# Optimization experiments

Hardware: AMD Instinct MI355X
Metric: run time of the kernel (lower is better)

Reference implementation:

```python
import jax, jax.numpy as jnp
import numpy as np

K = 50          # number of negative samples (init arg k)
GAMMA = 1.0     # margin (init arg gamma)
CHUNK = 32      # anchor-row chunk for cdist to bound memory


def cdist_l1(queries, base):
    """Pairwise cityblock distance [A, N] computed in chunks over queries."""
    A, d = queries.shape
    q = queries.reshape(A // CHUNK, CHUNK, d)

    def body(carry, q_chunk):
        # [CHUNK, N]
        dist = jnp.sum(jnp.abs(q_chunk[:, None, :] - base[None, :, :]), axis=-1)
        return carry, dist

    _, dists = jax.lax.scan(body, None, q)
    return dists.reshape(A, base.shape[0])


def setup_inputs() -> dict:
    key = jax.random.key(0)
    k1, k2, k3, k4 = jax.random.split(key, 4)
    N, d, A = 20000, 128, 1024
    return {
        "out1": jax.random.normal(k1, (N, d), dtype=jnp.float32),
        "out2": jax.random.normal(k2, (N, d), dtype=jnp.float32),
        "anchor1": jax.random.randint(k3, (A,), 0, N, dtype=jnp.int64),
        "anchor2": jax.random.randint(k4, (A,), 0, N, dtype=jnp.int64),
    }


def reference(out1, out2, anchor1, anchor2):
    ae1 = out1[anchor1]  # [A, d]
    ae2 = out2[anchor2]  # [A, d]

    # Negative sampling (torch does this on detached numpy arrays):
    # k nearest (smallest L1 distance) candidates in the other graph.
    o1s = jax.lax.stop_gradient(out1)
    o2s = jax.lax.stop_gradient(out2)
    dist1 = cdist_l1(jax.lax.stop_gradient(ae1), o2s)  # [A, N]
    dist2 = cdist_l1(jax.lax.stop_gradient(ae2), o1s)  # [A, N]
    _, neg_idx1 = jax.lax.top_k(-dist1, K)  # [A, K] indices into out2
    _, neg_idx2 = jax.lax.top_k(-dist2, K)  # [A, K] indices into out1

    neg1 = out2[neg_idx1]  # [A, K, d]
    neg2 = out1[neg_idx2]  # [A, K, d]

    pos = jnp.sum(jnp.abs(ae1 - ae2), axis=1)  # [A]
    D = pos + GAMMA

    B1 = -jnp.sum(jnp.abs(ae1[:, None, :] - neg1), axis=2)  # [A, K]
    L1 = jnp.sum(jax.nn.relu(D[:, None] + B1))
    B2 = -jnp.sum(jnp.abs(ae2[:, None, :] - neg2), axis=2)  # [A, K]
    L2 = jnp.sum(jax.nn.relu(D[:, None] + B2))

    return (L1 + L2) / (anchor1.shape[0] * K)
```

## Files before the change

kernel.cpp:

```cpp
#include <hip/hip_runtime.h>
#include <hip/hip_bf16.h>

#define NPTS  20000
#define DIM   128
#define NA    1024
#define NTASK 2048
#define G     8
#define P     4
#define TILE  1024
#define NTILE 20
#define NBX   (NTASK / G)
#define NWG   (NBX * NTILE)
#define SLOT  96
#define KSEL  50
#define GAMMA 1.0f
#define RRANK 12
#define LMAX  (NTILE * SLOT)
#define MFIX  8.0f
#define SQF   (255.0f / (2.0f * MFIX))
#define DQF   (2.0f * MFIX / 255.0f)
#define PRE_A (2 * NPTS * 8)
#define PRE_B (NTASK * 8)
#define PRE_N (PRE_A + PRE_B + 256)

typedef unsigned char  u8t;
typedef unsigned short u16t;

static __device__ __forceinline__ unsigned sad8(unsigned a, unsigned b, unsigned c) {
#if __has_builtin(__builtin_amdgcn_sad_u8)
    return __builtin_amdgcn_sad_u8(a, b, c);
#else
    unsigned d;
    asm("v_sad_u8 %0, %1, %2, %3" : "=v"(d) : "v"(a), "v"(b), "v"(c));
    return d;
#endif
}

static __device__ __forceinline__ unsigned q4(const float4 v, const float s) {
    unsigned u0 = __float2uint_rn(fminf(fmaxf((v.x + MFIX) * s, 0.0f), 255.0f));
    unsigned u1 = __float2uint_rn(fminf(fmaxf((v.y + MFIX) * s, 0.0f), 255.0f));
    unsigned u2 = __float2uint_rn(fminf(fmaxf((v.z + MFIX) * s, 0.0f), 255.0f));
    unsigned u3 = __float2uint_rn(fminf(fmaxf((v.w + MFIX) * s, 0.0f), 255.0f));
    return u0 | (u1 << 8) | (u2 << 16) | (u3 << 24);
}

__global__ __launch_bounds__(256) void prep_kernel(
    const float* __restrict__ o1, const float* __restrict__ o2,
    const int* __restrict__ anchor1, const int* __restrict__ anchor2,
    uint4* __restrict__ qp1, uint4* __restrict__ qp2,
    uint4* __restrict__ astage, float* __restrict__ out)
{
    const int idx = (int)blockIdx.x * 256 + (int)threadIdx.x;
    if (idx < PRE_A) {
        const int m  = idx / (NPTS * 8);
        const int r  = idx - m * (NPTS * 8);
        const int n  = r >> 3;
        const int cq = r & 7;
        const float4* src = (const float4*)((m ? o2 : o1) + (size_t)n * DIM + cq * 16);
        uint4 o;
        o.x = q4(src[0], SQF); o.y = q4(src[1], SQF);
        o.z = q4(src[2], SQF); o.w = q4(src[3], SQF);
        (m ? qp2 : qp1)[(size_t)cq * NPTS + n] = o;
    } else if (idx < PRE_A + PRE_B) {
        const int j = idx - PRE_A;
        const int t = j >> 3, cq = j & 7;
        int row; const float* src;
        if (t < NA) { row = anchor1[t];      src = o1; }
        else        { row = anchor2[t - NA]; src = o2; }
        const float4* rp = (const float4*)(src + (size_t)row * DIM + cq * 16);
        uint4 o;
        o.x = q4(rp[0], SQF); o.y = q4(rp[1], SQF);
        o.z = q4(rp[2], SQF); o.w = q4(rp[3], SQF);
        astage[(size_t)cq * NTASK + t] = o;
    } else if (idx == PRE_A + PRE_B) {
        out[0] = 0.0f;
    }
}

__global__ __launch_bounds__(256) void sample_kernel(
    const uint4* __restrict__ qp1, const uint4* __restrict__ qp2,
    const uint4* __restrict__ astage, unsigned* __restrict__ tau)
{
    __shared__ unsigned h[256], scn[256];
    __shared__ unsigned s_b0, s_r1;

    const int tid = threadIdx.x;
    const int t = (int)blockIdx.x;
    const uint4* qp = (t < NA) ? qp2 : qp1;

    uint4 A[8];
    #pragma unroll
    for (int cq = 0; cq < 8; ++cq) A[cq] = astage[(size_t)cq * NTASK + t];

    unsigned d[2];
    #pragma unroll
    for (int k = 0; k < 2; ++k) {
        const int s = tid + k * 256;
        const int n = (s >> 6) * 2500 + (s & 63);
        unsigned acc = 0;
        #pragma unroll
        for (int cq = 0; cq < 8; ++cq) {
            const uint4 pv = qp[(size_t)cq * NPTS + n];
            acc = sad8(pv.x, A[cq].x, acc); acc = sad8(pv.y, A[cq].y, acc);
            acc = sad8(pv.z, A[cq].z, acc); acc = sad8(pv.w, A[cq].w, acc);
        }
        d[k] = acc;
    }
    h[tid] = 0u;
    __syncthreads();
    atomicAdd(&h[d[0] >> 8], 1u);
    atomicAdd(&h[d[1] >> 8], 1u);
    __syncthreads();
    scn[tid] = h[tid];
    __syncthreads();
    for (int off = 1; off < 256; off <<= 1) {
        const unsigned v = scn[tid];
        const unsigned u = (tid >= off) ? scn[tid - off] : 0u;
        __syncthreads();
        scn[tid] = v + u;
        __syncthreads();
    }
    {
        const unsigned cumb = tid ? scn[tid - 1] : 0u;
        if (cumb < RRANK && scn[tid] >= RRANK) { s_b0 = (unsigned)tid; s_r1 = RRANK - cumb; }
    }
    __syncthreads();
    const unsigned b0 = s_b0, r1 = s_r1;
    h[tid] = 0u;
    __syncthreads();
    if ((d[0] >> 8) == b0) atomicAdd(&h[d[0] & 255u], 1u);
    if ((d[1] >> 8) == b0) atomicAdd(&h[d[1] & 255u], 1u);
    __syncthreads();
    scn[tid] = h[tid];
    __syncthreads();
    for (int off = 1; off < 256; off <<= 1) {
        const unsigned v = scn[tid];
        const unsigned u = (tid >= off) ? scn[tid - off] : 0u;
        __syncthreads();
        scn[tid] = v + u;
        __syncthreads();
    }
    {
        const unsigned cumb = tid ? scn[tid - 1] : 0u;
        if (cumb < r1 && scn[tid] >= r1) tau[t] = (b0 << 8) | (unsigned)tid;
    }
}

__global__ __launch_bounds__(256, 8) void dist_kernel(
    const uint4* __restrict__ qp1, const uint4* __restrict__ qp2,
    const uint4* __restrict__ astage, const unsigned* __restrict__ tau,
    u16t* __restrict__ cand, unsigned* __restrict__ bcnt)
{
    __shared__ unsigned scnt[G];

    const int tid = threadIdx.x;
    const int bid = (int)blockIdx.x;
    const int swz = (bid & 7) * (NWG / 8) + (bid >> 3);
    const int tile = swz / NBX;
    const int bx   = swz - tile * NBX;
    const int t0 = bx * G;
    const uint4* qp = (t0 < NA) ? qp2 : qp1;

    if (tid < G) scnt[tid] = 0u;

    const int w = tid >> 6, l = tid & 63;
    const int nbase = tile * TILE + w * 256 + l;

    unsigned acc[P][G];
    #pragma unroll
    for (int p = 0; p < P; ++p)
        #pragma unroll
        for (int g = 0; g < G; ++g) acc[p][g] = 0u;

    #pragma unroll
    for (int cq = 0; cq < 8; ++cq) {
        uint4 A[G];
        #pragma unroll
        for (int g = 0; g < G; ++g) A[g] = astage[(size_t)cq * NTASK + t0 + g];
        uint4 pv[P];
        #pragma unroll
        for (int p = 0; p < P; ++p) {
            int n = nbase + p * 64;
            n = n < NPTS ? n : NPTS - 1;
            pv[p] = qp[(size_t)cq * NPTS + n];
        }
        #pragma unroll
        for (int g = 0; g < G; ++g) {
            #pragma unroll
            for (int p = 0; p < P; ++p) {
                unsigned a = acc[p][g];
                a = sad8(pv[p].x, A[g].x, a);
                a = sad8(pv[p].y, A[g].y, a);
                a = sad8(pv[p].z, A[g].z, a);
                a = sad8(pv[p].w, A[g].w, a);
                acc[p][g] = a;
            }
        }
    }
    __syncthreads();

    #pragma unroll
    for (int g = 0; g < G; ++g) {
        const unsigned tg = tau[t0 + g];
        u16t* cg = cand + (size_t)(t0 + g) * LMAX + tile * SLOT;
        #pragma unroll
        for (int p = 0; p < P; ++p) {
            const int n = nbase + p * 64;
            if (n < NPTS && acc[p][g] <= tg) {
                const unsigned idx = atomicAdd(&scnt[g], 1u);
                if (idx < SLOT) cg[idx] = (u16t)acc[p][g];
            }
        }
    }
    __syncthreads();
    if (tid < G) bcnt[(size_t)(t0 + tid) * NTILE + tile] = scnt[tid];
}

__global__ __launch_bounds__(256) void finish_kernel(
    const float* __restrict__ o1, const float* __restrict__ o2,
    const int* __restrict__ anchor1, const int* __restrict__ anchor2,
    const uint4* __restrict__ qp1, const uint4* __restrict__ qp2,
    const uint4* __restrict__ astage,
    const u16t* __restrict__ cand, const unsigned* __restrict__ bcnt,
    float* __restrict__ d_out)
{
    __shared__ float red[256];
    __shared__ unsigned h[256], scn[256];
    __shared__ unsigned cnts[NTILE];
    __shared__ unsigned s_b0, s_r1, s_bad;

    const int tid = threadIdx.x;
    const int t = (int)blockIdx.x;

    const int a = (t < NA) ? t : (t - NA);
    const int i1 = anchor1[a], i2 = anchor2[a];
    float p = 0.0f;
    if (tid < DIM) p = fabsf(o1[(size_t)i1 * DIM + tid] - o2[(size_t)i2 * DIM + tid]);
    red[tid] = p;
    __syncthreads();
    for (int s = 128; s >= 1; s >>= 1) { if (tid < s) red[tid] += red[tid + s]; __syncthreads(); }
    const float D = red[0] + GAMMA;
    __syncthreads();

    if (tid < NTILE) cnts[tid] = bcnt[(size_t)t * NTILE + tid];
    __syncthreads();
    if (tid == 0) {
        unsigned total = 0, bad = 0;
        for (int i = 0; i < NTILE; ++i) { if (cnts[i] > SLOT) bad = 1; total += cnts[i]; }
        s_bad = bad | (total < KSEL ? 1u : 0u);
    }
    h[tid] = 0u;
    __syncthreads();

    float local = 0.0f;
    unsigned kth, remf;

    if (!s_bad) {
        const unsigned* c32 = (const unsigned*)(cand + (size_t)t * LMAX);
        unsigned val[8];
        #pragma unroll
        for (int k = 0; k < 4; ++k) {
            const int i32 = tid + k * 256;
            unsigned v0 = 0xFFFFu, v1 = 0xFFFFu;
            if (i32 < LMAX / 2) {
                const unsigned wv = c32[i32];
                const int tile = i32 / (SLOT / 2);
                const int j0 = 2 * i32 - tile * SLOT;
                const unsigned cn = cnts[tile];
                if ((unsigned)j0 < cn)       v0 = wv & 0xFFFFu;
                if ((unsigned)(j0 + 1) < cn) v1 = wv >> 16;
            }
            val[2 * k] = v0; val[2 * k + 1] = v1;
            if (v0 != 0xFFFFu) atomicAdd(&h[v0 >> 8], 1u);
            if (v1 != 0xFFFFu) atomicAdd(&h[v1 >> 8], 1u);
        }
        __syncthreads();
        scn[tid] = h[tid];
        __syncthreads();
        for (int off = 1; off < 256; off <<= 1) {
            const unsigned v = scn[tid];
            const unsigned u = (tid >= off) ? scn[tid - off] : 0u;
            __syncthreads();
            scn[tid] = v + u;
            __syncthreads();
        }
        {
            const unsigned cumb = tid ? scn[tid - 1] : 0u;
            if (cumb < KSEL && scn[tid] >= KSEL) { s_b0 = (unsigned)tid; s_r1 = KSEL - cumb; }
        }
        __syncthreads();
        const unsigned b0 = s_b0, r1 = s_r1;
        h[tid] = 0u;
        __syncthreads();
        #pragma unroll
        for (int k = 0; k < 8; ++k)
            if ((val[k] >> 8) == b0) atomicAdd(&h[val[k] & 255u], 1u);
        __syncthreads();
        scn[tid] = h[tid];
        __syncthreads();
        for (int off = 1; off < 256; off <<= 1) {
            const unsigned v = scn[tid];
            const unsigned u = (tid >= off) ? scn[tid - off] : 0u;
            __syncthreads();
            scn[tid] = v + u;
            __syncthreads();
        }
        {
            const unsigned cumb = tid ? scn[tid - 1] : 0u;
            if (cumb < r1 && scn[tid] >= r1) { s_b0 = (unsigned)tid; s_r1 = r1 - cumb; }
        }
        __syncthreads();
        kth = (b0 << 8) | s_b0;
        remf = s_r1;
        #pragma unroll
        for (int k = 0; k < 8; ++k) {
            const unsigned u = val[k];
            if (u < kth) local += fmaxf(D - (float)u * DQF, 0.0f);
        }
    } else {
        const uint4* qp = (t < NA) ? qp2 : qp1;
        uint4 A[8];
        #pragma unroll
        for (int cq = 0; cq < 8; ++cq) A[cq] = astage[(size_t)cq * NTASK + t];
        for (int n = tid; n < NPTS; n += 256) {
            unsigned acc = 0;
            #pragma unroll
            for (int cq = 0; cq < 8; ++cq) {
                const uint4 pv = qp[(size_t)cq * NPTS + n];
                acc = sad8(pv.x, A[cq].x, acc); acc = sad8(pv.y, A[cq].y, acc);
                acc = sad8(pv.z, A[cq].z, acc); acc = sad8(pv.w, A[cq].w, acc);
            }
            atomicAdd(&h[acc >> 8], 1u);
        }
        __syncthreads();
        scn[tid] = h[tid];
        __syncthreads();
        for (int off = 1; off < 256; off <<= 1) {
            const unsigned v = scn[tid];
            const unsigned u = (tid >= off) ? scn[tid - off] : 0u;
            __syncthreads();
            scn[tid] = v + u;
            __syncthreads();
        }
        {
            const unsigned cumb = tid ? scn[tid - 1] : 0u;
            if (cumb < KSEL && scn[tid] >= KSEL) { s_b0 = (unsigned)tid; s_r1 = KSEL - cumb; }
        }
        __syncthreads();
        const unsigned b0 = s_b0, r1 = s_r1;
        h[tid] = 0u;
        __syncthreads();
        for (int n = tid; n < NPTS; n += 256) {
            unsigned acc = 0;
            #pragma unroll
            for (int cq = 0; cq < 8; ++cq) {
                const uint4 pv = qp[(size_t)cq * NPTS + n];
                acc = sad8(pv.x, A[cq].x, acc); acc = sad8(pv.y, A[cq].y, acc);
                acc = sad8(pv.z, A[cq].z, acc); acc = sad8(pv.w, A[cq].w, acc);
            }
            if ((acc >> 8) == b0) atomicAdd(&h[acc & 255u], 1u);
        }
        __syncthreads();
        scn[tid] = h[tid];
        __syncthreads();
        for (int off = 1; off < 256; off <<= 1) {
            const unsigned v = scn[tid];
            const unsigned u = (tid >= off) ? scn[tid - off] : 0u;
            __syncthreads();
            scn[tid] = v + u;
            __syncthreads();
        }
        {
            const unsigned cumb = tid ? scn[tid - 1] : 0u;
            if (cumb < r1 && scn[tid] >= r1) { s_b0 = (unsigned)tid; s_r1 = r1 - cumb; }
        }
        __syncthreads();
        kth = (b0 << 8) | s_b0;
        remf = s_r1;
        for (int n = tid; n < NPTS; n += 256) {
            unsigned acc = 0;
            #pragma unroll
            for (int cq = 0; cq < 8; ++cq) {
                const uint4 pv = qp[(size_t)cq * NPTS + n];
                acc = sad8(pv.x, A[cq].x, acc); acc = sad8(pv.y, A[cq].y, acc);
                acc = sad8(pv.z, A[cq].z, acc); acc = sad8(pv.w, A[cq].w, acc);
            }
            if (acc < kth) local += fmaxf(D - (float)acc * DQF, 0.0f);
        }
    }

    red[tid] = local;
    __syncthreads();
    for (int s = 128; s >= 1; s >>= 1) { if (tid < s) red[tid] += red[tid + s]; __syncthreads(); }
    if (tid == 0) {
        const float total_l = red[0] + (float)remf * fmaxf(D - (float)kth * DQF, 0.0f);
        atomicAdd(d_out, total_l * (1.0f / ((float)NA * (float)KSEL)));
    }
}

extern "C" void kernel_launch(void* const* d_in, const int* in_sizes, int n_in,
                              void* d_out, int out_size, void* d_ws, size_t ws_size,
                              hipStream_t stream) {
    const float* o1 = (const float*)d_in[0];
    const float* o2 = (const float*)d_in[1];
    const int*   a1 = (const int*)d_in[2];
    const int*   a2 = (const int*)d_in[3];
    float* out = (float*)d_out;

    const size_t qbytes = (size_t)NPTS * DIM;
    const size_t abytes = (size_t)NTASK * DIM;
    const uintptr_t end = ((uintptr_t)d_ws + ws_size) & ~(uintptr_t)15;
    unsigned* tau    = (unsigned*)(end - (size_t)NTASK * 4);
    unsigned* bcnt   = (unsigned*)((uintptr_t)tau - (size_t)NTASK * NTILE * 4);
    uint4*    astage = (uint4*)((uintptr_t)bcnt - abytes);
    uint4*    qp2    = (uint4*)((uintptr_t)astage - qbytes);
    uint4*    qp1    = (uint4*)((uintptr_t)qp2 - qbytes);
    u16t*     cand   = (u16t*)d_ws;

    prep_kernel<<<(PRE_N + 255) / 256, 256, 0, stream>>>(
        o1, o2, a1, a2, qp1, qp2, astage, out);
    sample_kernel<<<NTASK, 256, 0, stream>>>(qp1, qp2, astage, tau);
    dist_kernel<<<NWG, 256, 0, stream>>>(qp1, qp2, astage, tau, cand, bcnt);
    finish_kernel<<<NTASK, 256, 0, stream>>>(o1, o2, a1, a2, qp1, qp2, astage,
                                             cand, bcnt, out);
}
```

Baseline: 110.9 us.

## Fuse quantization prep into sampling kernel by quantizing sample rows on the fly

Merges the prep kernel and the sample kernel into one launch. Extra blocks do the quantization while the sampling blocks quantize their anchor and sampled base rows directly from the float inputs, so sampling no longer waits on the prep output. This removes one launch and the serialization between the two stages, at the cost of redundant quantization arithmetic and wider float reads in the sampling blocks. A second, small change in finish_kernel only loads a candidate word when at least one of its two slots is valid.

```diff
diff --git a/kernel.cpp b/kernel.cpp
--- a/kernel.cpp
+++ b/kernel.cpp
@@ -22,6 +22,8 @@
 #define PRE_A (2 * NPTS * 8)
 #define PRE_B (NTASK * 8)
 #define PRE_N (PRE_A + PRE_B + 256)
+#define PBLK  ((PRE_N + 255) / 256)
+#define FUSED (NTASK + PBLK)
 
 typedef unsigned char  u8t;
 typedef unsigned short u16t;
@@ -44,63 +46,78 @@
     return u0 | (u1 << 8) | (u2 << 16) | (u3 << 24);
 }
 
-__global__ __launch_bounds__(256) void prep_kernel(
+__global__ __launch_bounds__(256) void prep_sample_kernel(
     const float* __restrict__ o1, const float* __restrict__ o2,
     const int* __restrict__ anchor1, const int* __restrict__ anchor2,
     uint4* __restrict__ qp1, uint4* __restrict__ qp2,
-    uint4* __restrict__ astage, float* __restrict__ out)
-{
-    const int idx = (int)blockIdx.x * 256 + (int)threadIdx.x;
-    if (idx < PRE_A) {
-        const int m  = idx / (NPTS * 8);
-        const int r  = idx - m * (NPTS * 8);
-        const int n  = r >> 3;
-        const int cq = r & 7;
-        const float4* src = (const float4*)((m ? o2 : o1) + (size_t)n * DIM + cq * 16);
-        uint4 o;
-        o.x = q4(src[0], SQF); o.y = q4(src[1], SQF);
-        o.z = q4(src[2], SQF); o.w = q4(src[3], SQF);
-        (m ? qp2 : qp1)[(size_t)cq * NPTS + n] = o;
-    } else if (idx < PRE_A + PRE_B) {
-        const int j = idx - PRE_A;
-        const int t = j >> 3, cq = j & 7;
-        int row; const float* src;
-        if (t < NA) { row = anchor1[t];      src = o1; }
-        else        { row = anchor2[t - NA]; src = o2; }
-        const float4* rp = (const float4*)(src + (size_t)row * DIM + cq * 16);
-        uint4 o;
-        o.x = q4(rp[0], SQF); o.y = q4(rp[1], SQF);
-        o.z = q4(rp[2], SQF); o.w = q4(rp[3], SQF);
-        astage[(size_t)cq * NTASK + t] = o;
-    } else if (idx == PRE_A + PRE_B) {
-        out[0] = 0.0f;
-    }
-}
-
-__global__ __launch_bounds__(256) void sample_kernel(
-    const uint4* __restrict__ qp1, const uint4* __restrict__ qp2,
-    const uint4* __restrict__ astage, unsigned* __restrict__ tau)
+    uint4* __restrict__ astage, unsigned* __restrict__ tau,
+    float* __restrict__ out)
 {
     __shared__ unsigned h[256], scn[256];
     __shared__ unsigned s_b0, s_r1;
 
     const int tid = threadIdx.x;
-    const int t = (int)blockIdx.x;
-    const uint4* qp = (t < NA) ? qp2 : qp1;
-
+    const int bid = (int)blockIdx.x;
+
+    if (bid >= NTASK) {
+        const int idx = (bid - NTASK) * 256 + tid;
+        if (idx < PRE_A) {
+            const int m  = idx / (NPTS * 8);
+            const int r  = idx - m * (NPTS * 8);
+            const int n  = r >> 3;
+            const int cq = r & 7;
+            const float4* src = (const float4*)((m ? o2 : o1) + (size_t)n * DIM + cq * 16);
+            uint4 o;
+            o.x = q4(src[0], SQF); o.y = q4(src[1], SQF);
+            o.z = q4(src[2], SQF); o.w = q4(src[3], SQF);
+            (m ? qp2 : qp1)[(size_t)cq * NPTS + n] = o;
+        } else if (idx < PRE_A + PRE_B) {
+            const int j = idx - PRE_A;
+            const int t = j >> 3, cq = j & 7;
+            int row; const float* src;
+            if (t < NA) { row = anchor1[t];      src = o1; }
+            else        { row = anchor2[t - NA]; src = o2; }
+            const float4* rp = (const float4*)(src + (size_t)row * DIM + cq * 16);
+            uint4 o;
+            o.x = q4(rp[0], SQF); o.y = q4(rp[1], SQF);
+            o.z = q4(rp[2], SQF); o.w = q4(rp[3], SQF);
+            astage[(size_t)cq * NTASK + t] = o;
+        } else if (idx == PRE_A + PRE_B) {
+            out[0] = 0.0f;
+        }
+        return;
+    }
+
+    const int t = bid;
+    const float* base = (t < NA) ? o2 : o1;
+
+    int row; const float* asrc;
+    if (t < NA) { row = anchor1[t];      asrc = o1; }
+    else        { row = anchor2[t - NA]; asrc = o2; }
+    const float4* ap = (const float4*)(asrc + (size_t)row * DIM);
     uint4 A[8];
     #pragma unroll
-    for (int cq = 0; cq < 8; ++cq) A[cq] = astage[(size_t)cq * NTASK + t];
+    for (int cq = 0; cq < 8; ++cq) {
+        A[cq].x = q4(ap[4 * cq + 0], SQF);
+        A[cq].y = q4(ap[4 * cq + 1], SQF);
+        A[cq].z = q4(ap[4 * cq + 2], SQF);
+        A[cq].w = q4(ap[4 * cq + 3], SQF);
+    }
 
     unsigned d[2];
     #pragma unroll
     for (int k = 0; k < 2; ++k) {
         const int s = tid + k * 256;
         const int n = (s >> 6) * 2500 + (s & 63);
+        const float4* rp = (const float4*)(base + (size_t)n * DIM);
         unsigned acc = 0;
         #pragma unroll
         for (int cq = 0; cq < 8; ++cq) {
-            const uint4 pv = qp[(size_t)cq * NPTS + n];
+            uint4 pv;
+            pv.x = q4(rp[4 * cq + 0], SQF);
+            pv.y = q4(rp[4 * cq + 1], SQF);
+            pv.z = q4(rp[4 * cq + 2], SQF);
+            pv.w = q4(rp[4 * cq + 3], SQF);
             acc = sad8(pv.x, A[cq].x, acc); acc = sad8(pv.y, A[cq].y, acc);
             acc = sad8(pv.z, A[cq].z, acc); acc = sad8(pv.w, A[cq].w, acc);
         }
@@ -263,12 +280,14 @@
             const int i32 = tid + k * 256;
             unsigned v0 = 0xFFFFu, v1 = 0xFFFFu;
             if (i32 < LMAX / 2) {
-                const unsigned wv = c32[i32];
                 const int tile = i32 / (SLOT / 2);
                 const int j0 = 2 * i32 - tile * SLOT;
                 const unsigned cn = cnts[tile];
-                if ((unsigned)j0 < cn)       v0 = wv & 0xFFFFu;
-                if ((unsigned)(j0 + 1) < cn) v1 = wv >> 16;
+                if ((unsigned)j0 < cn) {
+                    const unsigned wv = c32[i32];
+                    v0 = wv & 0xFFFFu;
+                    if ((unsigned)(j0 + 1) < cn) v1 = wv >> 16;
+                }
             }
             val[2 * k] = v0; val[2 * k + 1] = v1;
             if (v0 != 0xFFFFu) atomicAdd(&h[v0 >> 8], 1u);
@@ -417,9 +436,8 @@
     uint4*    qp1    = (uint4*)((uintptr_t)qp2 - qbytes);
     u16t*     cand   = (u16t*)d_ws;
 
-    prep_kernel<<<(PRE_N + 255) / 256, 256, 0, stream>>>(
-        o1, o2, a1, a2, qp1, qp2, astage, out);
-    sample_kernel<<<NTASK, 256, 0, stream>>>(qp1, qp2, astage, tau);
+    prep_sample_kernel<<<FUSED, 256, 0, stream>>>(
+        o1, o2, a1, a2, qp1, qp2, astage, tau, out);
     dist_kernel<<<NWG, 256, 0, stream>>>(qp1, qp2, astage, tau, cand, bcnt);
     finish_kernel<<<NTASK, 256, 0, stream>>>(o1, o2, a1, a2, qp1, qp2, astage,
                                              cand, bcnt, out);
```

New measurement: 176.3 us. 59.0% more time.
